# Performance work log

Measured on AMD Instinct MI355X. Metric: run time of the kernel, lower is better.

## Reference

```python
import jax, jax.numpy as jnp
import numpy as np

# Dimensions (source globals scaled to production: r=256 residues, s=128 sequences)
S, R, CM, CZ, C, H = 128, 256, 256, 128, 32, 8
EPS = 1e-5  # torch LayerNorm default


def setup_inputs() -> dict:
    key = jax.random.key(0)
    ks = jax.random.split(key, 14)
    msa = jax.random.normal(ks[0], (S, R, CM), dtype=jnp.float32)
    pair = jax.random.normal(ks[1], (R, R, CZ), dtype=jnp.float32)
    u = lambda k, shape, fan: jax.random.uniform(k, shape, jnp.float32, -1.0 / np.sqrt(fan), 1.0 / np.sqrt(fan))
    return {
        "msa": msa,
        "pair": pair,
        # per-head LayerNorm affine params (stacked over head axis)
        "ln_msa_g": 1.0 + 0.1 * jax.random.normal(ks[2], (H, CM), dtype=jnp.float32),
        "ln_msa_b": 0.1 * jax.random.normal(ks[3], (H, CM), dtype=jnp.float32),
        "ln_pair_g": 1.0 + 0.1 * jax.random.normal(ks[4], (H, CZ), dtype=jnp.float32),
        "ln_pair_b": 0.1 * jax.random.normal(ks[5], (H, CZ), dtype=jnp.float32),
        # per-head projections (torch Linear without bias; stored as (in, out))
        "Wq": u(ks[6], (H, CM, C), CM),
        "Wk": u(ks[7], (H, CM, C), CM),
        "Wv": u(ks[8], (H, CM, C), CM),
        "Wg": u(ks[9], (H, CM, C), CM),
        "Wb": u(ks[10], (H, CZ, S), CZ),  # linear_b: c_z -> s
        # output projection c*H -> c_m (with bias)
        "Wo": u(ks[11], (H * C, CM), H * C),
        "bo": u(ks[12], (CM,), H * C),
    }


def _forward(msa, pair, ln_msa_g, ln_msa_b, ln_pair_g, ln_pair_b, Wq, Wk, Wv, Wg, Wb, Wo, bo):
    # LayerNorm normalization is head-independent; only affine differs per head.
    mu = msa.mean(-1, keepdims=True)
    var = msa.var(-1, keepdims=True)
    nm = (msa - mu) * jax.lax.rsqrt(var + EPS)              # (S, R, CM)
    p = nm[None] * ln_msa_g[:, None, None, :] + ln_msa_b[:, None, None, :]  # (H, S, R, CM)

    q = jnp.einsum("hsrc,hcd->hsrd", p, Wq)                  # (H, S, R, C)
    k = jnp.einsum("hsrc,hcd->hsrd", p, Wk)
    v = jnp.einsum("hsrc,hcd->hsrd", p, Wv)
    g = jax.nn.sigmoid(jnp.einsum("hsrc,hcd->hsrd", p, Wg))

    pmu = pair.mean(-1, keepdims=True)
    pvar = pair.var(-1, keepdims=True)
    npair = (pair - pmu) * jax.lax.rsqrt(pvar + EPS)         # (R, R, CZ)
    pp = npair[None] * ln_pair_g[:, None, None, :] + ln_pair_b[:, None, None, :]  # (H, R, R, CZ)
    bflat = jnp.einsum("hijc,hcs->hijs", pp, Wb)             # (H, R, R, S)
    # Faithful to torch: b = linear_b(flat_pair).view(s, r, r) -- a raw
    # row-major reinterpretation (NOT a transpose).
    b = bflat.reshape(H, S, R, R)

    inv_sqrt_c = np.float32(1.0 / np.sqrt(C))
    scores = (jnp.einsum("hsid,hsjd->hsij", q, k) + b) * inv_sqrt_c  # (H, S, R, R)
    # Source softmax is over dim=-2 (the query/row axis), faithful here.
    a = jax.nn.softmax(scores, axis=-2)
    o = g * jnp.einsum("hsij,hsjd->hsid", a, v)              # (H, S, R, C)

    # concat heads on last dim: (S, R, H*C)
    cat = jnp.transpose(o, (1, 2, 0, 3)).reshape(S, R, H * C)
    return cat @ Wo + bo                                      # (S, R, CM)


def reference(msa, pair, ln_msa_g, ln_msa_b, ln_pair_g, ln_pair_b, Wq, Wk, Wv, Wg, Wb, Wo, bo):
    return _forward(msa, pair, ln_msa_g, ln_msa_b, ln_pair_g, ln_pair_b, Wq, Wk, Wv, Wg, Wb, Wo, bo)
```

## Files before the change

### kernel.cpp

```cpp
#include <hip/hip_runtime.h>
#include <hip/hip_bf16.h>


namespace {
constexpr int S_ = 128, R_ = 256, CM_ = 256, CZ_ = 128, C_ = 32, H_ = 8;
constexpr int SR_ = S_ * R_;
constexpr int RR_ = R_ * R_;
constexpr float EPS_ = 1e-5f;
constexpr float ISC_ = 0.17677669529663687f;

constexpr size_t OFF_WC  = 0;
constexpr size_t OFF_BC  = 131072;
constexpr size_t OFF_BBP = 132096;
constexpr size_t F32_END = 133120;
constexpr size_t BF_BASE = F32_END * 4;
constexpr size_t QKVG_ELEMS  = (size_t)H_ * SR_ * C_;
constexpr size_t CAT_ELEMS   = (size_t)SR_ * CM_;
constexpr size_t WBT_ELEMS   = (size_t)H_ * 128 * 128;
constexpr size_t WOT_ELEMS   = (size_t)256 * 256;
constexpr size_t PAIRN_ELEMS = (size_t)RR_ * 128;
constexpr size_t MSAN_ELEMS  = (size_t)SR_ * 256;
constexpr size_t NEED_BYTES =
    BF_BASE +
    (4 * QKVG_ELEMS + CAT_ELEMS + WBT_ELEMS + WOT_ELEMS + PAIRN_ELEMS + MSAN_ELEMS) * 2;
}

typedef unsigned short bf_t;
typedef short s8v __attribute__((ext_vector_type(8)));
typedef float f4v __attribute__((ext_vector_type(4)));

__device__ __forceinline__ unsigned pk2(float lo, float hi) {
  __hip_bfloat162 t = __float22bfloat162_rn(float2{lo, hi});
  return *reinterpret_cast<unsigned*>(&t);
}
__device__ __forceinline__ bf_t pk1(float v) {
  __hip_bfloat16 t = __float2bfloat16(v);
  return *reinterpret_cast<bf_t*>(&t);
}
__device__ __forceinline__ float uplo(unsigned u) { return __uint_as_float(u << 16); }
__device__ __forceinline__ f4v mfma16(s8v a, s8v b, f4v c) {
  return __builtin_amdgcn_mfma_f32_16x16x32_bf16(a, b, c, 0, 0, 0);
}
__device__ __forceinline__ s8v ld8(const bf_t* p) { return *reinterpret_cast<const s8v*>(p); }

__global__ __launch_bounds__(512) void prep_all_k(
    const float* __restrict__ pair, const float* __restrict__ msa,
    const float* __restrict__ lng_m, const float* __restrict__ lnb_m,
    const float* __restrict__ lng_p, const float* __restrict__ lnb_p,
    const float* __restrict__ Wq, const float* __restrict__ Wk, const float* __restrict__ Wv,
    const float* __restrict__ Wg, const float* __restrict__ Wb, const float* __restrict__ Wo,
    bf_t* __restrict__ pairN, bf_t* __restrict__ msaN, bf_t* __restrict__ wct,
    bf_t* __restrict__ wbt, bf_t* __restrict__ wot, float* __restrict__ bc,
    float* __restrict__ bbp) {
  int b = blockIdx.x;
  int tid = threadIdx.x;
  int lane = tid & 63;
  if (b < 8192) {
    int row = b * 8 + (tid >> 6);
    float2 v = reinterpret_cast<const float2*>(pair + (size_t)row * CZ_)[lane];
    float s = v.x + v.y;
    float s2 = v.x * v.x + v.y * v.y;
    for (int off = 32; off; off >>= 1) {
      s += __shfl_xor(s, off);
      s2 += __shfl_xor(s2, off);
    }
    float m = s / CZ_;
    float rs = rsqrtf(s2 / CZ_ - m * m + EPS_);
    reinterpret_cast<unsigned*>(pairN)[(size_t)row * 64 + lane] =
        pk2((v.x - m) * rs, (v.y - m) * rs);
  } else if (b < 12288) {
    int row = (b - 8192) * 8 + (tid >> 6);
    float4 v = reinterpret_cast<const float4*>(msa + (size_t)row * CM_)[lane];
    float s = v.x + v.y + v.z + v.w;
    float s2 = v.x * v.x + v.y * v.y + v.z * v.z + v.w * v.w;
    for (int off = 32; off; off >>= 1) {
      s += __shfl_xor(s, off);
      s2 += __shfl_xor(s2, off);
    }
    float m = s / CM_;
    float rs = rsqrtf(s2 / CM_ - m * m + EPS_);
    uint2 wv;
    wv.x = pk2((v.x - m) * rs, (v.y - m) * rs);
    wv.y = pk2((v.z - m) * rs, (v.w - m) * rs);
    reinterpret_cast<uint2*>(msaN)[(size_t)row * 64 + lane] = wv;
  } else if (b < 13184) {
    int idx = (b - 12288) * 512 + tid;
    if (idx < 262144) {
      int h = idx >> 15, rem = idx & 32767;
      int j = rem >> 8, c = rem & 255;
      int m = j >> 5, d = j & 31;
      const float* Wsrc = (m == 0) ? Wq : (m == 1) ? Wk : (m == 2) ? Wv : Wg;
      float scale = (m == 0) ? ISC_ : 1.0f;
      wct[idx] = pk1(lng_m[h * CM_ + c] * Wsrc[((size_t)h * CM_ + c) * C_ + d] * scale);
    } else if (idx < 262144 + 131072) {
      int i2 = idx - 262144;
      int h = i2 >> 14, rem = i2 & 16383;
      int t = rem >> 7, c = rem & 127;
      wbt[i2] = pk1(lng_p[h * CZ_ + c] * Wb[((size_t)h * CZ_ + c) * S_ + t] * ISC_);
    } else {
      int i3 = idx - 262144 - 131072;
      int n = i3 >> 8, k = i3 & 255;
      wot[i3] = pk1(Wo[(size_t)k * 256 + n]);
    }
  } else {
    int ob = (b - 13184) * 4 + (tid >> 7);
    int t = tid & 127;
    if (ob < H_) {
      int h = ob;
      int m = t >> 5, d = t & 31;
      const float* Wsrc = (m == 0) ? Wq : (m == 1) ? Wk : (m == 2) ? Wv : Wg;
      float scale = (m == 0) ? ISC_ : 1.0f;
      float bias = 0.f;
      for (int c = 0; c < CM_; c++)
        bias += lnb_m[h * CM_ + c] * Wsrc[((size_t)h * CM_ + c) * C_ + d];
      bc[h * 128 + t] = bias * scale;
    } else {
      int h = ob - H_;
      float bias = 0.f;
      for (int c = 0; c < CZ_; c++)
        bias += lnb_p[h * CZ_ + c] * Wb[((size_t)h * CZ_ + c) * S_ + t];
      bbp[h * 128 + t] = bias * ISC_;
    }
  }
}

__global__ __launch_bounds__(512, 1) void qkvg_mfma_k(
    const bf_t* __restrict__ msaN, const bf_t* __restrict__ wct, const float* __restrict__ bc,
    bf_t* __restrict__ q, bf_t* __restrict__ k, bf_t* __restrict__ v, bf_t* __restrict__ g) {
  __shared__ bf_t sm_a[128 * 256];
  __shared__ bf_t sm_w[128 * 256];
  int ib = blockIdx.x;
  int tid = threadIdx.x;
  int w = tid >> 6, l = tid & 63;
  int l15 = l & 15, l4 = l >> 4;
  int iw = w >> 2, jw = w & 3;
  int sr0 = ib * 128;
  int sx7 = l15 & 7;
#pragma unroll
  for (int rep = 0; rep < 8; rep++) {
    int flat = rep * 512 + tid;
    int row = flat >> 5, c = flat & 31;
    *reinterpret_cast<uint4*>(&sm_a[row * 256 + ((c ^ (row & 7)) << 3)]) =
        *reinterpret_cast<const uint4*>(msaN + (size_t)(sr0 + row) * 256 + c * 8);
  }
  for (int h = 0; h < H_; h++) {
    __syncthreads();
#pragma unroll
    for (int rep = 0; rep < 8; rep++) {
      int flat = rep * 512 + tid;
      int row = flat >> 5, c = flat & 31;
      *reinterpret_cast<uint4*>(&sm_w[row * 256 + ((c ^ (row & 7)) << 3)]) =
          *reinterpret_cast<const uint4*>(wct + ((size_t)h * 128 + row) * 256 + c * 8);
    }
    f4v acc[4][2];
#pragma unroll
    for (int jt = 0; jt < 2; jt++) {
      float bb = bc[h * 128 + jw * 32 + jt * 16 + l15];
#pragma unroll
      for (int it = 0; it < 4; it++) acc[it][jt] = f4v{bb, bb, bb, bb};
    }
    __syncthreads();
#pragma unroll
    for (int ks = 0; ks < 8; ks++) {
      int ch = ks * 4 + l4;
      s8v a[4], b[2];
#pragma unroll
      for (int it = 0; it < 4; it++)
        a[it] = ld8(&sm_a[(iw * 64 + it * 16 + l15) * 256 + ((ch ^ sx7) << 3)]);
#pragma unroll
      for (int jt = 0; jt < 2; jt++)
        b[jt] = ld8(&sm_w[(jw * 32 + jt * 16 + l15) * 256 + ((ch ^ sx7) << 3)]);
#pragma unroll
      for (int it = 0; it < 4; it++)
#pragma unroll
        for (int jt = 0; jt < 2; jt++) acc[it][jt] = mfma16(a[it], b[jt], acc[it][jt]);
    }
#pragma unroll
    for (int it = 0; it < 4; it++) {
#pragma unroll
      for (int jt = 0; jt < 2; jt++) {
        int j = jw * 32 + jt * 16 + l15;
        int m_ = j >> 5, d = j & 31;
        bf_t* dst = (m_ == 0) ? q : (m_ == 1) ? k : (m_ == 2) ? v : g;
#pragma unroll
        for (int r = 0; r < 4; r++) {
          int i = iw * 64 + it * 16 + l4 * 4 + r;
          float val = acc[it][jt][r];
          if (m_ == 3) val = 1.f / (1.f + __expf(-val));
          dst[((size_t)h * SR_ + sr0 + i) * C_ + d] = pk1(val);
        }
      }
    }
  }
}

__global__ __launch_bounds__(512, 1) void attn_mfma_k(
    const bf_t* __restrict__ pairN, const bf_t* __restrict__ wbt,
    const float* __restrict__ bbp, const bf_t* __restrict__ qg, const bf_t* __restrict__ kg,
    const bf_t* __restrict__ vg, const bf_t* __restrict__ gg, bf_t* __restrict__ cat) {
  __shared__ bf_t sm_pN[256 * 128];
  __shared__ bf_t sm_wt[64 * 128];
  __shared__ bf_t sm_p[256 * 64];
  __shared__ bf_t sm_vt[32 * 64];
  __shared__ float sm_redm[4 * 64];
  __shared__ float sm_reds[4 * 64];

  int b = blockIdx.x;
  int x = b & 7, t = b >> 3;
  int round = t >> 5, inner = t & 31;
  int sl = inner >> 3, h = inner & 7;
  int s = (round * 8 + x) * 4 + sl;

  int tid = threadIdx.x;
  int w = tid >> 6, l = tid & 63;
  int l15 = l & 15, l4 = l >> 4;
  int iw = w >> 1, jw = w & 1;
  int iw2 = w >> 1, dw = w & 1;
  int sx7 = l15 & 7;
  size_t base = ((size_t)h * SR_ + (size_t)s * R_) * C_;

  s8v qa[4];
#pragma unroll
  for (int it = 0; it < 4; it++)
    qa[it] = ld8(&qg[base + (size_t)(iw * 64 + it * 16 + l15) * C_ + l4 * 8]);

  f4v accO[4];
#pragma unroll
  for (int it = 0; it < 4; it++) accO[it] = f4v{0.f, 0.f, 0.f, 0.f};

  for (int p = 0; p < 2; p++) {
    __syncthreads();
#pragma unroll
    for (int rep = 0; rep < 8; rep++) {
      int flat = rep * 512 + tid;
      int row = flat >> 4, c = flat & 15;
      int gr = (2 * s + (row >> 7)) * 256 + 2 * (row & 127) + p;
      *reinterpret_cast<uint4*>(&sm_pN[row * 128 + ((c ^ (row & 7)) << 3)]) =
          *reinterpret_cast<const uint4*>(pairN + (size_t)gr * 128 + c * 8);
    }
    for (int jh = 0; jh < 2; jh++) {
      int j0 = p * 128 + jh * 64;
      s8v kb0 = ld8(&kg[base + (size_t)(j0 + jw * 32 + l15) * C_ + l4 * 8]);
      s8v kb1 = ld8(&kg[base + (size_t)(j0 + jw * 32 + 16 + l15) * C_ + l4 * 8]);
      __syncthreads();
      if (tid < 256) {
#pragma unroll
        for (int rep = 0; rep < 4; rep++) {
          int flat = rep * 256 + tid;
          int row = flat >> 4, c = flat & 15;
          *reinterpret_cast<uint4*>(&sm_wt[row * 128 + ((c ^ (row & 7)) << 3)]) =
              *reinterpret_cast<const uint4*>(wbt + ((size_t)h * 128 + jh * 64 + row) * 128 +
                                              c * 8);
        }
      } else {
        int t2 = tid - 256;
        int j = t2 >> 2, dc = t2 & 3;
        uint4 u = *reinterpret_cast<const uint4*>(vg + base + (size_t)(j0 + j) * C_ + dc * 8);
        unsigned uu[4] = {u.x, u.y, u.z, u.w};
#pragma unroll
        for (int e = 0; e < 8; e++) {
          int d = dc * 8 + e;
          bf_t val = (bf_t)((uu[e >> 1] >> ((e & 1) * 16)) & 0xffff);
          sm_vt[d * 64 + ((((j >> 3) ^ (d & 7)) << 3) + (j & 7))] = val;
        }
      }
      f4v acc[4][2];
      {
        float bb0 = bbp[h * 128 + jh * 64 + jw * 32 + l15];
        float bb1 = bbp[h * 128 + jh * 64 + jw * 32 + 16 + l15];
#pragma unroll
        for (int it = 0; it < 4; it++) {
          acc[it][0] = f4v{bb0, bb0, bb0, bb0};
          acc[it][1] = f4v{bb1, bb1, bb1, bb1};
        }
      }
      __syncthreads();
#pragma unroll
      for (int ks = 0; ks < 4; ks++) {
        int ch = (ks * 4 + l4);
        s8v a[4], b2[2];
#pragma unroll
        for (int it = 0; it < 4; it++)
          a[it] = ld8(&sm_pN[(iw * 64 + it * 16 + l15) * 128 + ((ch ^ sx7) << 3)]);
#pragma unroll
        for (int u = 0; u < 2; u++)
          b2[u] = ld8(&sm_wt[(jw * 32 + u * 16 + l15) * 128 + ((ch ^ sx7) << 3)]);
#pragma unroll
        for (int it = 0; it < 4; it++) {
          acc[it][0] = mfma16(a[it], b2[0], acc[it][0]);
          acc[it][1] = mfma16(a[it], b2[1], acc[it][1]);
        }
      }
#pragma unroll
      for (int it = 0; it < 4; it++) {
        acc[it][0] = mfma16(qa[it], kb0, acc[it][0]);
        acc[it][1] = mfma16(qa[it], kb1, acc[it][1]);
      }
      float fac[2], mloc[2];
#pragma unroll
      for (int u = 0; u < 2; u++) {
        float m0 = -1e30f;
#pragma unroll
        for (int it = 0; it < 4; it++)
#pragma unroll
          for (int r = 0; r < 4; r++) m0 = fmaxf(m0, acc[it][u][r]);
        m0 = fmaxf(m0, __shfl_xor(m0, 16));
        m0 = fmaxf(m0, __shfl_xor(m0, 32));
        float s0 = 0.f;
#pragma unroll
        for (int it = 0; it < 4; it++)
#pragma unroll
          for (int r = 0; r < 4; r++) {
            float e = __expf(acc[it][u][r] - m0);
            acc[it][u][r] = e;
            s0 += e;
          }
        s0 += __shfl_xor(s0, 16);
        s0 += __shfl_xor(s0, 32);
        mloc[u] = m0;
        if (l < 16) {
          sm_redm[iw * 64 + jw * 32 + u * 16 + l] = m0;
          sm_reds[iw * 64 + jw * 32 + u * 16 + l] = s0;
        }
      }
      __syncthreads();
#pragma unroll
      for (int u = 0; u < 2; u++) {
        int jc = jw * 32 + u * 16 + l15;
        float M = fmaxf(fmaxf(sm_redm[jc], sm_redm[64 + jc]),
                        fmaxf(sm_redm[128 + jc], sm_redm[192 + jc]));
        float tot = 0.f;
#pragma unroll
        for (int gx = 0; gx < 4; gx++)
          tot += sm_reds[gx * 64 + jc] * __expf(sm_redm[gx * 64 + jc] - M);
        fac[u] = __expf(mloc[u] - M) / tot;
#pragma unroll
        for (int it = 0; it < 4; it++)
#pragma unroll
          for (int r = 0; r < 4; r++) {
            int i = iw * 64 + it * 16 + l4 * 4 + r;
            sm_p[i * 64 + ((((jc >> 3) ^ (i & 7)) << 3) + (jc & 7))] =
                pk1(acc[it][u][r] * fac[u]);
          }
      }
      __syncthreads();
#pragma unroll
      for (int ks = 0; ks < 2; ks++) {
        int ch = ks * 4 + l4;
        s8v vb = ld8(&sm_vt[(dw * 16 + l15) * 64 + ((ch ^ sx7) << 3)]);
#pragma unroll
        for (int it = 0; it < 4; it++) {
          s8v pa = ld8(&sm_p[(iw2 * 64 + it * 16 + l15) * 64 + ((ch ^ sx7) << 3)]);
          accO[it] = mfma16(pa, vb, accO[it]);
        }
      }
    }
  }
#pragma unroll
  for (int it = 0; it < 4; it++) {
#pragma unroll
    for (int r = 0; r < 4; r++) {
      int i = iw2 * 64 + it * 16 + l4 * 4 + r;
      int d = dw * 16 + l15;
      float gf = uplo((unsigned)gg[base + (size_t)i * C_ + d]);
      cat[((size_t)s * R_ + i) * 256 + h * 32 + d] = pk1(accO[it][r] * gf);
    }
  }
}

__global__ __launch_bounds__(512, 1) void out_mfma_k(const bf_t* __restrict__ cat,
                                                     const bf_t* __restrict__ wot,
                                                     const float* __restrict__ bo,
                                                     float* __restrict__ out) {
  __shared__ bf_t sm_a[128 * 256];
  __shared__ bf_t sm_b[128 * 256];
  int ib = blockIdx.x;
  int tid = threadIdx.x;
  int w = tid >> 6, l = tid & 63;
  int l15 = l & 15, l4 = l >> 4, sx7 = l15 & 7;
  int iw = w >> 2, jw = w & 3;
  int sr0 = ib * 128;
#pragma unroll
  for (int rep = 0; rep < 8; rep++) {
    int flat = rep * 512 + tid;
    int row = flat >> 5, c = flat & 31;
    *reinterpret_cast<uint4*>(&sm_a[row * 256 + ((c ^ (row & 7)) << 3)]) =
        *reinterpret_cast<const uint4*>(cat + (size_t)(sr0 + row) * 256 + c * 8);
  }
  for (int nb = 0; nb < 2; nb++) {
    __syncthreads();
#pragma unroll
    for (int rep = 0; rep < 8; rep++) {
      int flat = rep * 512 + tid;
      int row = flat >> 5, c = flat & 31;
      *reinterpret_cast<uint4*>(&sm_b[row * 256 + ((c ^ (row & 7)) << 3)]) =
          *reinterpret_cast<const uint4*>(wot + (size_t)(nb * 128 + row) * 256 + c * 8);
    }
    f4v acc[4][2];
#pragma unroll
    for (int jt = 0; jt < 2; jt++) {
      float bb = bo[nb * 128 + jw * 32 + jt * 16 + l15];
#pragma unroll
      for (int it = 0; it < 4; it++) acc[it][jt] = f4v{bb, bb, bb, bb};
    }
    __syncthreads();
#pragma unroll
    for (int ks = 0; ks < 8; ks++) {
      int ch = ks * 4 + l4;
      s8v a[4], b[2];
#pragma unroll
      for (int it = 0; it < 4; it++)
        a[it] = ld8(&sm_a[(iw * 64 + it * 16 + l15) * 256 + ((ch ^ sx7) << 3)]);
#pragma unroll
      for (int jt = 0; jt < 2; jt++)
        b[jt] = ld8(&sm_b[(jw * 32 + jt * 16 + l15) * 256 + ((ch ^ sx7) << 3)]);
#pragma unroll
      for (int it = 0; it < 4; it++)
#pragma unroll
        for (int jt = 0; jt < 2; jt++) acc[it][jt] = mfma16(a[it], b[jt], acc[it][jt]);
    }
#pragma unroll
    for (int it = 0; it < 4; it++)
#pragma unroll
      for (int jt = 0; jt < 2; jt++) {
        int n = nb * 128 + jw * 32 + jt * 16 + l15;
#pragma unroll
        for (int r = 0; r < 4; r++) {
          int i = iw * 64 + it * 16 + l4 * 4 + r;
          out[(size_t)(sr0 + i) * 256 + n] = acc[it][jt][r];
        }
      }
  }
}

extern "C" void kernel_launch(void* const* d_in, const int* in_sizes, int n_in, void* d_out,
                              int out_size, void* d_ws, size_t ws_size, hipStream_t stream) {
  if (ws_size < NEED_BYTES) return;

  const float* msa = (const float*)d_in[0];
  const float* pair = (const float*)d_in[1];
  const float* lng_m = (const float*)d_in[2];
  const float* lnb_m = (const float*)d_in[3];
  const float* lng_p = (const float*)d_in[4];
  const float* lnb_p = (const float*)d_in[5];
  const float* Wq = (const float*)d_in[6];
  const float* Wk = (const float*)d_in[7];
  const float* Wv = (const float*)d_in[8];
  const float* Wg = (const float*)d_in[9];
  const float* Wb = (const float*)d_in[10];
  const float* Wo = (const float*)d_in[11];
  const float* bo = (const float*)d_in[12];
  float* out = (float*)d_out;
  float* ws = (float*)d_ws;

  bf_t* wct = (bf_t*)(ws + OFF_WC);
  float* bc = ws + OFF_BC;
  float* bbp = ws + OFF_BBP;
  bf_t* qb = (bf_t*)((char*)d_ws + BF_BASE);
  bf_t* kb = qb + QKVG_ELEMS;
  bf_t* vb = kb + QKVG_ELEMS;
  bf_t* gb = vb + QKVG_ELEMS;
  bf_t* cat = gb + QKVG_ELEMS;
  bf_t* wbt = cat + CAT_ELEMS;
  bf_t* wot = wbt + WBT_ELEMS;
  bf_t* pairN = wot + WOT_ELEMS;
  bf_t* msaN = pairN + PAIRN_ELEMS;

  prep_all_k<<<13188, 512, 0, stream>>>(pair, msa, lng_m, lnb_m, lng_p, lnb_p, Wq, Wk, Wv, Wg,
                                        Wb, Wo, pairN, msaN, wct, wbt, wot, bc, bbp);
  qkvg_mfma_k<<<SR_ / 128, 512, 0, stream>>>(msaN, wct, bc, qb, kb, vb, gb);
  attn_mfma_k<<<S_ * H_, 512, 0, stream>>>(pairN, wbt, bbp, qb, kb, vb, gb, cat);
  out_mfma_k<<<SR_ / 128, 512, 0, stream>>>(cat, wot, bo, out);
}
```

Measured before the change: 159.5 us.

## Shrink attention LDS footprint via K-chunked pair staging to raise occupancy

The attention kernel now stages the normalized pair tile and the Wb slice in two 64-channel K chunks instead of the full 128 channels. This cuts LDS use from about 96KB to about 48KB per block, and launch bounds are raised to allow more resident blocks per CU. The price is reloading the pair tile for every 64-column pass instead of once per 128-row parity, plus extra barriers. The prep kernel also moves the slow serial bias-reduction blocks to the front of the grid so they start early.

```diff
diff --git a/kernel.cpp b/kernel.cpp
--- a/kernel.cpp
+++ b/kernel.cpp
@@ -55,8 +55,27 @@
   int b = blockIdx.x;
   int tid = threadIdx.x;
   int lane = tid & 63;
-  if (b < 8192) {
-    int row = b * 8 + (tid >> 6);
+  if (b < 4) {
+    int ob = b * 4 + (tid >> 7);
+    int t = tid & 127;
+    if (ob < H_) {
+      int h = ob;
+      int m = t >> 5, d = t & 31;
+      const float* Wsrc = (m == 0) ? Wq : (m == 1) ? Wk : (m == 2) ? Wv : Wg;
+      float scale = (m == 0) ? ISC_ : 1.0f;
+      float bias = 0.f;
+      for (int c = 0; c < CM_; c++)
+        bias += lnb_m[h * CM_ + c] * Wsrc[((size_t)h * CM_ + c) * C_ + d];
+      bc[h * 128 + t] = bias * scale;
+    } else {
+      int h = ob - H_;
+      float bias = 0.f;
+      for (int c = 0; c < CZ_; c++)
+        bias += lnb_p[h * CZ_ + c] * Wb[((size_t)h * CZ_ + c) * S_ + t];
+      bbp[h * 128 + t] = bias * ISC_;
+    }
+  } else if (b < 8196) {
+    int row = (b - 4) * 8 + (tid >> 6);
     float2 v = reinterpret_cast<const float2*>(pair + (size_t)row * CZ_)[lane];
     float s = v.x + v.y;
     float s2 = v.x * v.x + v.y * v.y;
@@ -68,8 +87,8 @@
     float rs = rsqrtf(s2 / CZ_ - m * m + EPS_);
     reinterpret_cast<unsigned*>(pairN)[(size_t)row * 64 + lane] =
         pk2((v.x - m) * rs, (v.y - m) * rs);
-  } else if (b < 12288) {
-    int row = (b - 8192) * 8 + (tid >> 6);
+  } else if (b < 12292) {
+    int row = (b - 8196) * 8 + (tid >> 6);
     float4 v = reinterpret_cast<const float4*>(msa + (size_t)row * CM_)[lane];
     float s = v.x + v.y + v.z + v.w;
     float s2 = v.x * v.x + v.y * v.y + v.z * v.z + v.w * v.w;
@@ -83,8 +102,8 @@
     wv.x = pk2((v.x - m) * rs, (v.y - m) * rs);
     wv.y = pk2((v.z - m) * rs, (v.w - m) * rs);
     reinterpret_cast<uint2*>(msaN)[(size_t)row * 64 + lane] = wv;
-  } else if (b < 13184) {
-    int idx = (b - 12288) * 512 + tid;
+  } else {
+    int idx = (b - 12292) * 512 + tid;
     if (idx < 262144) {
       int h = idx >> 15, rem = idx & 32767;
       int j = rem >> 8, c = rem & 255;
@@ -102,25 +121,6 @@
       int n = i3 >> 8, k = i3 & 255;
       wot[i3] = pk1(Wo[(size_t)k * 256 + n]);
     }
-  } else {
-    int ob = (b - 13184) * 4 + (tid >> 7);
-    int t = tid & 127;
-    if (ob < H_) {
-      int h = ob;
-      int m = t >> 5, d = t & 31;
-      const float* Wsrc = (m == 0) ? Wq : (m == 1) ? Wk : (m == 2) ? Wv : Wg;
-      float scale = (m == 0) ? ISC_ : 1.0f;
-      float bias = 0.f;
-      for (int c = 0; c < CM_; c++)
-        bias += lnb_m[h * CM_ + c] * Wsrc[((size_t)h * CM_ + c) * C_ + d];
-      bc[h * 128 + t] = bias * scale;
-    } else {
-      int h = ob - H_;
-      float bias = 0.f;
-      for (int c = 0; c < CZ_; c++)
-        bias += lnb_p[h * CZ_ + c] * Wb[((size_t)h * CZ_ + c) * S_ + t];
-      bbp[h * 128 + t] = bias * ISC_;
-    }
   }
 }
 
@@ -194,30 +194,29 @@
   }
 }
 
-__global__ __launch_bounds__(512, 1) void attn_mfma_k(
+__global__ __launch_bounds__(512, 4) void attn_mfma_k(
     const bf_t* __restrict__ pairN, const bf_t* __restrict__ wbt,
     const float* __restrict__ bbp, const bf_t* __restrict__ qg, const bf_t* __restrict__ kg,
     const bf_t* __restrict__ vg, const bf_t* __restrict__ gg, bf_t* __restrict__ cat) {
-  __shared__ bf_t sm_pN[256 * 128];
-  __shared__ bf_t sm_wt[64 * 128];
+  __shared__ bf_t sm_pn[256 * 64];
+  __shared__ bf_t sm_wt[64 * 64];
   __shared__ bf_t sm_p[256 * 64];
   __shared__ bf_t sm_vt[32 * 64];
   __shared__ float sm_redm[4 * 64];
   __shared__ float sm_reds[4 * 64];
 
   int b = blockIdx.x;
-  int x = b & 7, t = b >> 3;
-  int round = t >> 5, inner = t & 31;
+  int x = b & 7, tq = b >> 3;
+  int round = tq >> 5, inner = tq & 31;
   int sl = inner >> 3, h = inner & 7;
   int s = (round * 8 + x) * 4 + sl;
 
   int tid = threadIdx.x;
   int w = tid >> 6, l = tid & 63;
-  int l15 = l & 15, l4 = l >> 4;
-  int iw = w >> 1, jw = w & 1;
-  int iw2 = w >> 1, dw = w & 1;
-  int sx7 = l15 & 7;
+  int l15 = l & 15, l4 = l >> 4, sx7 = l15 & 7;
+  int iw = w >> 1, jw = w & 1, dw = w & 1;
   size_t base = ((size_t)h * SR_ + (size_t)s * R_) * C_;
+  const bf_t* wbh = wbt + (size_t)h * 128 * 128;
 
   s8v qa[4];
 #pragma unroll
@@ -228,131 +227,130 @@
 #pragma unroll
   for (int it = 0; it < 4; it++) accO[it] = f4v{0.f, 0.f, 0.f, 0.f};
 
-  for (int p = 0; p < 2; p++) {
-    __syncthreads();
-#pragma unroll
-    for (int rep = 0; rep < 8; rep++) {
-      int flat = rep * 512 + tid;
-      int row = flat >> 4, c = flat & 15;
-      int gr = (2 * s + (row >> 7)) * 256 + 2 * (row & 127) + p;
-      *reinterpret_cast<uint4*>(&sm_pN[row * 128 + ((c ^ (row & 7)) << 3)]) =
-          *reinterpret_cast<const uint4*>(pairN + (size_t)gr * 128 + c * 8);
-    }
-    for (int jh = 0; jh < 2; jh++) {
-      int j0 = p * 128 + jh * 64;
-      s8v kb0 = ld8(&kg[base + (size_t)(j0 + jw * 32 + l15) * C_ + l4 * 8]);
-      s8v kb1 = ld8(&kg[base + (size_t)(j0 + jw * 32 + 16 + l15) * C_ + l4 * 8]);
+  for (int pass = 0; pass < 4; pass++) {
+    int p = pass >> 1, jh = pass & 1;
+    int j0 = p * 128 + jh * 64;
+    s8v kb0 = ld8(&kg[base + (size_t)(j0 + jw * 32 + l15) * C_ + l4 * 8]);
+    s8v kb1 = ld8(&kg[base + (size_t)(j0 + jw * 32 + 16 + l15) * C_ + l4 * 8]);
+    __syncthreads();
+    if (tid >= 256) {
+      int t2 = tid - 256;
+      int j = t2 >> 2, dc = t2 & 3;
+      uint4 u = *reinterpret_cast<const uint4*>(vg + base + (size_t)(j0 + j) * C_ + dc * 8);
+      unsigned uu[4] = {u.x, u.y, u.z, u.w};
+#pragma unroll
+      for (int e = 0; e < 8; e++) {
+        int d = dc * 8 + e;
+        bf_t val = (bf_t)((uu[e >> 1] >> ((e & 1) * 16)) & 0xffff);
+        sm_vt[d * 64 + ((((j >> 3) ^ (d & 7)) << 3) + (j & 7))] = val;
+      }
+    }
+    f4v acc[4][2];
+    {
+      float bb0 = bbp[h * 128 + jh * 64 + jw * 32 + l15];
+      float bb1 = bbp[h * 128 + jh * 64 + jw * 32 + 16 + l15];
+#pragma unroll
+      for (int it = 0; it < 4; it++) {
+        acc[it][0] = f4v{bb0, bb0, bb0, bb0};
+        acc[it][1] = f4v{bb1, bb1, bb1, bb1};
+      }
+    }
+#pragma unroll
+    for (int kc = 0; kc < 2; kc++) {
+#pragma unroll
+      for (int rep = 0; rep < 4; rep++) {
+        int idx = rep * 512 + tid;
+        int row = idx >> 3, c8 = idx & 7;
+        int gr = (2 * s + (row >> 7)) * 256 + 2 * (row & 127) + p;
+        *reinterpret_cast<uint4*>(&sm_pn[row * 64 + ((c8 ^ (row & 7)) << 3)]) =
+            *reinterpret_cast<const uint4*>(pairN + (size_t)gr * 128 + kc * 64 + c8 * 8);
+      }
+      {
+        int row = tid >> 3, c8 = tid & 7;
+        *reinterpret_cast<uint4*>(&sm_wt[row * 64 + ((c8 ^ (row & 7)) << 3)]) =
+            *reinterpret_cast<const uint4*>(wbh + (size_t)(jh * 64 + row) * 128 + kc * 64 +
+                                            c8 * 8);
+      }
       __syncthreads();
-      if (tid < 256) {
-#pragma unroll
-        for (int rep = 0; rep < 4; rep++) {
-          int flat = rep * 256 + tid;
-          int row = flat >> 4, c = flat & 15;
-          *reinterpret_cast<uint4*>(&sm_wt[row * 128 + ((c ^ (row & 7)) << 3)]) =
-              *reinterpret_cast<const uint4*>(wbt + ((size_t)h * 128 + jh * 64 + row) * 128 +
-                                              c * 8);
-        }
-      } else {
-        int t2 = tid - 256;
-        int j = t2 >> 2, dc = t2 & 3;
-        uint4 u = *reinterpret_cast<const uint4*>(vg + base + (size_t)(j0 + j) * C_ + dc * 8);
-        unsigned uu[4] = {u.x, u.y, u.z, u.w};
-#pragma unroll
-        for (int e = 0; e < 8; e++) {
-          int d = dc * 8 + e;
-          bf_t val = (bf_t)((uu[e >> 1] >> ((e & 1) * 16)) & 0xffff);
-          sm_vt[d * 64 + ((((j >> 3) ^ (d & 7)) << 3) + (j & 7))] = val;
-        }
-      }
-      f4v acc[4][2];
-      {
-        float bb0 = bbp[h * 128 + jh * 64 + jw * 32 + l15];
-        float bb1 = bbp[h * 128 + jh * 64 + jw * 32 + 16 + l15];
-#pragma unroll
-        for (int it = 0; it < 4; it++) {
-          acc[it][0] = f4v{bb0, bb0, bb0, bb0};
-          acc[it][1] = f4v{bb1, bb1, bb1, bb1};
-        }
-      }
-      __syncthreads();
-#pragma unroll
-      for (int ks = 0; ks < 4; ks++) {
-        int ch = (ks * 4 + l4);
+#pragma unroll
+      for (int ks = 0; ks < 2; ks++) {
+        int ch = ks * 4 + l4;
         s8v a[4], b2[2];
 #pragma unroll
         for (int it = 0; it < 4; it++)
-          a[it] = ld8(&sm_pN[(iw * 64 + it * 16 + l15) * 128 + ((ch ^ sx7) << 3)]);
+          a[it] = ld8(&sm_pn[(iw * 64 + it * 16 + l15) * 64 + ((ch ^ sx7) << 3)]);
 #pragma unroll
         for (int u = 0; u < 2; u++)
-          b2[u] = ld8(&sm_wt[(jw * 32 + u * 16 + l15) * 128 + ((ch ^ sx7) << 3)]);
+          b2[u] = ld8(&sm_wt[(jw * 32 + u * 16 + l15) * 64 + ((ch ^ sx7) << 3)]);
 #pragma unroll
         for (int it = 0; it < 4; it++) {
           acc[it][0] = mfma16(a[it], b2[0], acc[it][0]);
           acc[it][1] = mfma16(a[it], b2[1], acc[it][1]);
         }
       }
+      if (kc == 0) __syncthreads();
+    }
+#pragma unroll
+    for (int it = 0; it < 4; it++) {
+      acc[it][0] = mfma16(qa[it], kb0, acc[it][0]);
+      acc[it][1] = mfma16(qa[it], kb1, acc[it][1]);
+    }
+    float fac[2], mloc[2];
+#pragma unroll
+    for (int u = 0; u < 2; u++) {
+      float m0 = -1e30f;
+#pragma unroll
+      for (int it = 0; it < 4; it++)
+#pragma unroll
+        for (int r = 0; r < 4; r++) m0 = fmaxf(m0, acc[it][u][r]);
+      m0 = fmaxf(m0, __shfl_xor(m0, 16));
+      m0 = fmaxf(m0, __shfl_xor(m0, 32));
+      float s0 = 0.f;
+#pragma unroll
+      for (int it = 0; it < 4; it++)
+#pragma unroll
+        for (int r = 0; r < 4; r++) {
+          float e = __expf(acc[it][u][r] - m0);
+          acc[it][u][r] = e;
+          s0 += e;
+        }
+      s0 += __shfl_xor(s0, 16);
+      s0 += __shfl_xor(s0, 32);
+      mloc[u] = m0;
+      if (l < 16) {
+        sm_redm[iw * 64 + jw * 32 + u * 16 + l] = m0;
+        sm_reds[iw * 64 + jw * 32 + u * 16 + l] = s0;
+      }
+    }
+    __syncthreads();
+#pragma unroll
+    for (int u = 0; u < 2; u++) {
+      int jc = jw * 32 + u * 16 + l15;
+      float M = fmaxf(fmaxf(sm_redm[jc], sm_redm[64 + jc]),
+                      fmaxf(sm_redm[128 + jc], sm_redm[192 + jc]));
+      float tot = 0.f;
+#pragma unroll
+      for (int gx = 0; gx < 4; gx++)
+        tot += sm_reds[gx * 64 + jc] * __expf(sm_redm[gx * 64 + jc] - M);
+      fac[u] = __expf(mloc[u] - M) / tot;
+#pragma unroll
+      for (int it = 0; it < 4; it++)
+#pragma unroll
+        for (int r = 0; r < 4; r++) {
+          int i = iw * 64 + it * 16 + l4 * 4 + r;
+          sm_p[i * 64 + ((((jc >> 3) ^ (i & 7)) << 3) + (jc & 7))] =
+              pk1(acc[it][u][r] * fac[u]);
+        }
+    }
+    __syncthreads();
+#pragma unroll
+    for (int ks = 0; ks < 2; ks++) {
+      int ch = ks * 4 + l4;
+      s8v vb = ld8(&sm_vt[(dw * 16 + l15) * 64 + ((ch ^ sx7) << 3)]);
 #pragma unroll
       for (int it = 0; it < 4; it++) {
-        acc[it][0] = mfma16(qa[it], kb0, acc[it][0]);
-        acc[it][1] = mfma16(qa[it], kb1, acc[it][1]);
-      }
-      float fac[2], mloc[2];
-#pragma unroll
-      for (int u = 0; u < 2; u++) {
-        float m0 = -1e30f;
-#pragma unroll
-        for (int it = 0; it < 4; it++)
-#pragma unroll
-          for (int r = 0; r < 4; r++) m0 = fmaxf(m0, acc[it][u][r]);
-        m0 = fmaxf(m0, __shfl_xor(m0, 16));
-        m0 = fmaxf(m0, __shfl_xor(m0, 32));
-        float s0 = 0.f;
-#pragma unroll
-        for (int it = 0; it < 4; it++)
-#pragma unroll
-          for (int r = 0; r < 4; r++) {
-            float e = __expf(acc[it][u][r] - m0);
-            acc[it][u][r] = e;
-            s0 += e;
-          }
-        s0 += __shfl_xor(s0, 16);
-        s0 += __shfl_xor(s0, 32);
-        mloc[u] = m0;
-        if (l < 16) {
-          sm_redm[iw * 64 + jw * 32 + u * 16 + l] = m0;
-          sm_reds[iw * 64 + jw * 32 + u * 16 + l] = s0;
-        }
-      }
-      __syncthreads();
-#pragma unroll
-      for (int u = 0; u < 2; u++) {
-        int jc = jw * 32 + u * 16 + l15;
-        float M = fmaxf(fmaxf(sm_redm[jc], sm_redm[64 + jc]),
-                        fmaxf(sm_redm[128 + jc], sm_redm[192 + jc]));
-        float tot = 0.f;
-#pragma unroll
-        for (int gx = 0; gx < 4; gx++)
-          tot += sm_reds[gx * 64 + jc] * __expf(sm_redm[gx * 64 + jc] - M);
-        fac[u] = __expf(mloc[u] - M) / tot;
-#pragma unroll
-        for (int it = 0; it < 4; it++)
-#pragma unroll
-          for (int r = 0; r < 4; r++) {
-            int i = iw * 64 + it * 16 + l4 * 4 + r;
-            sm_p[i * 64 + ((((jc >> 3) ^ (i & 7)) << 3) + (jc & 7))] =
-                pk1(acc[it][u][r] * fac[u]);
-          }
-      }
-      __syncthreads();
-#pragma unroll
-      for (int ks = 0; ks < 2; ks++) {
-        int ch = ks * 4 + l4;
-        s8v vb = ld8(&sm_vt[(dw * 16 + l15) * 64 + ((ch ^ sx7) << 3)]);
-#pragma unroll
-        for (int it = 0; it < 4; it++) {
-          s8v pa = ld8(&sm_p[(iw2 * 64 + it * 16 + l15) * 64 + ((ch ^ sx7) << 3)]);
-          accO[it] = mfma16(pa, vb, accO[it]);
-        }
+        s8v pa = ld8(&sm_p[(iw * 64 + it * 16 + l15) * 64 + ((ch ^ sx7) << 3)]);
+        accO[it] = mfma16(pa, vb, accO[it]);
       }
     }
   }
@@ -360,7 +358,7 @@
   for (int it = 0; it < 4; it++) {
 #pragma unroll
     for (int r = 0; r < 4; r++) {
-      int i = iw2 * 64 + it * 16 + l4 * 4 + r;
+      int i = iw * 64 + it * 16 + l4 * 4 + r;
       int d = dw * 16 + l15;
       float gf = uplo((unsigned)gg[base + (size_t)i * C_ + d]);
       cat[((size_t)s * R_ + i) * 256 + h * 32 + d] = pk1(accO[it][r] * gf);
```

New measurement: 272.5 us. +70.8%, slower.

## Double attention block to 1024 threads and move bias blocks first in prep

Applied to the files above, without the earlier changes.

The attention kernel now runs 1024 threads (16 waves) per block. Each wave handles 32 query rows instead of 64, and the cross-wave softmax reduction spans 8 row groups. Loading of the Wb tile and the V transpose is redistributed across the larger thread count. Separately, the slow serial bias-dot-product blocks in the prep kernel are moved to the lowest block indices so they start first instead of trailing the launch. This is meant to add latency hiding and cut tail time, at the cost of more synchronisation participants and smaller MFMA tiles per wave.

```diff
diff --git a/kernel.cpp b/kernel.cpp
--- a/kernel.cpp
+++ b/kernel.cpp
@@ -55,8 +55,27 @@
   int b = blockIdx.x;
   int tid = threadIdx.x;
   int lane = tid & 63;
-  if (b < 8192) {
-    int row = b * 8 + (tid >> 6);
+  if (b < 4) {
+    int ob = b * 4 + (tid >> 7);
+    int t = tid & 127;
+    if (ob < H_) {
+      int h = ob;
+      int m = t >> 5, d = t & 31;
+      const float* Wsrc = (m == 0) ? Wq : (m == 1) ? Wk : (m == 2) ? Wv : Wg;
+      float scale = (m == 0) ? ISC_ : 1.0f;
+      float bias = 0.f;
+      for (int c = 0; c < CM_; c++)
+        bias += lnb_m[h * CM_ + c] * Wsrc[((size_t)h * CM_ + c) * C_ + d];
+      bc[h * 128 + t] = bias * scale;
+    } else {
+      int h = ob - H_;
+      float bias = 0.f;
+      for (int c = 0; c < CZ_; c++)
+        bias += lnb_p[h * CZ_ + c] * Wb[((size_t)h * CZ_ + c) * S_ + t];
+      bbp[h * 128 + t] = bias * ISC_;
+    }
+  } else if (b < 8196) {
+    int row = (b - 4) * 8 + (tid >> 6);
     float2 v = reinterpret_cast<const float2*>(pair + (size_t)row * CZ_)[lane];
     float s = v.x + v.y;
     float s2 = v.x * v.x + v.y * v.y;
@@ -68,8 +87,8 @@
     float rs = rsqrtf(s2 / CZ_ - m * m + EPS_);
     reinterpret_cast<unsigned*>(pairN)[(size_t)row * 64 + lane] =
         pk2((v.x - m) * rs, (v.y - m) * rs);
-  } else if (b < 12288) {
-    int row = (b - 8192) * 8 + (tid >> 6);
+  } else if (b < 12292) {
+    int row = (b - 8196) * 8 + (tid >> 6);
     float4 v = reinterpret_cast<const float4*>(msa + (size_t)row * CM_)[lane];
     float s = v.x + v.y + v.z + v.w;
     float s2 = v.x * v.x + v.y * v.y + v.z * v.z + v.w * v.w;
@@ -83,8 +102,8 @@
     wv.x = pk2((v.x - m) * rs, (v.y - m) * rs);
     wv.y = pk2((v.z - m) * rs, (v.w - m) * rs);
     reinterpret_cast<uint2*>(msaN)[(size_t)row * 64 + lane] = wv;
-  } else if (b < 13184) {
-    int idx = (b - 12288) * 512 + tid;
+  } else {
+    int idx = (b - 12292) * 512 + tid;
     if (idx < 262144) {
       int h = idx >> 15, rem = idx & 32767;
       int j = rem >> 8, c = rem & 255;
@@ -102,25 +121,6 @@
       int n = i3 >> 8, k = i3 & 255;
       wot[i3] = pk1(Wo[(size_t)k * 256 + n]);
     }
-  } else {
-    int ob = (b - 13184) * 4 + (tid >> 7);
-    int t = tid & 127;
-    if (ob < H_) {
-      int h = ob;
-      int m = t >> 5, d = t & 31;
-      const float* Wsrc = (m == 0) ? Wq : (m == 1) ? Wk : (m == 2) ? Wv : Wg;
-      float scale = (m == 0) ? ISC_ : 1.0f;
-      float bias = 0.f;
-      for (int c = 0; c < CM_; c++)
-        bias += lnb_m[h * CM_ + c] * Wsrc[((size_t)h * CM_ + c) * C_ + d];
-      bc[h * 128 + t] = bias * scale;
-    } else {
-      int h = ob - H_;
-      float bias = 0.f;
-      for (int c = 0; c < CZ_; c++)
-        bias += lnb_p[h * CZ_ + c] * Wb[((size_t)h * CZ_ + c) * S_ + t];
-      bbp[h * 128 + t] = bias * ISC_;
-    }
   }
 }
 
@@ -194,7 +194,7 @@
   }
 }
 
-__global__ __launch_bounds__(512, 1) void attn_mfma_k(
+__global__ __launch_bounds__(1024, 4) void attn_mfma_k(
     const bf_t* __restrict__ pairN, const bf_t* __restrict__ wbt,
     const float* __restrict__ bbp, const bf_t* __restrict__ qg, const bf_t* __restrict__ kg,
     const bf_t* __restrict__ vg, const bf_t* __restrict__ gg, bf_t* __restrict__ cat) {
@@ -202,37 +202,35 @@
   __shared__ bf_t sm_wt[64 * 128];
   __shared__ bf_t sm_p[256 * 64];
   __shared__ bf_t sm_vt[32 * 64];
-  __shared__ float sm_redm[4 * 64];
-  __shared__ float sm_reds[4 * 64];
+  __shared__ float sm_redm[8 * 64];
+  __shared__ float sm_reds[8 * 64];
 
   int b = blockIdx.x;
-  int x = b & 7, t = b >> 3;
-  int round = t >> 5, inner = t & 31;
+  int x = b & 7, tq = b >> 3;
+  int round = tq >> 5, inner = tq & 31;
   int sl = inner >> 3, h = inner & 7;
   int s = (round * 8 + x) * 4 + sl;
 
   int tid = threadIdx.x;
   int w = tid >> 6, l = tid & 63;
-  int l15 = l & 15, l4 = l >> 4;
-  int iw = w >> 1, jw = w & 1;
-  int iw2 = w >> 1, dw = w & 1;
-  int sx7 = l15 & 7;
+  int l15 = l & 15, l4 = l >> 4, sx7 = l15 & 7;
+  int iw = w >> 1, jw = w & 1, dw = w & 1;
   size_t base = ((size_t)h * SR_ + (size_t)s * R_) * C_;
 
-  s8v qa[4];
-#pragma unroll
-  for (int it = 0; it < 4; it++)
-    qa[it] = ld8(&qg[base + (size_t)(iw * 64 + it * 16 + l15) * C_ + l4 * 8]);
-
-  f4v accO[4];
-#pragma unroll
-  for (int it = 0; it < 4; it++) accO[it] = f4v{0.f, 0.f, 0.f, 0.f};
+  s8v qa[2];
+#pragma unroll
+  for (int it = 0; it < 2; it++)
+    qa[it] = ld8(&qg[base + (size_t)(iw * 32 + it * 16 + l15) * C_ + l4 * 8]);
+
+  f4v accO[2];
+#pragma unroll
+  for (int it = 0; it < 2; it++) accO[it] = f4v{0.f, 0.f, 0.f, 0.f};
 
   for (int p = 0; p < 2; p++) {
     __syncthreads();
 #pragma unroll
-    for (int rep = 0; rep < 8; rep++) {
-      int flat = rep * 512 + tid;
+    for (int rep = 0; rep < 4; rep++) {
+      int flat = rep * 1024 + tid;
       int row = flat >> 4, c = flat & 15;
       int gr = (2 * s + (row >> 7)) * 256 + 2 * (row & 127) + p;
       *reinterpret_cast<uint4*>(&sm_pN[row * 128 + ((c ^ (row & 7)) << 3)]) =
@@ -243,18 +241,14 @@
       s8v kb0 = ld8(&kg[base + (size_t)(j0 + jw * 32 + l15) * C_ + l4 * 8]);
       s8v kb1 = ld8(&kg[base + (size_t)(j0 + jw * 32 + 16 + l15) * C_ + l4 * 8]);
       __syncthreads();
+      {
+        int row = tid >> 4, c = tid & 15;
+        *reinterpret_cast<uint4*>(&sm_wt[row * 128 + ((c ^ (row & 7)) << 3)]) =
+            *reinterpret_cast<const uint4*>(wbt + ((size_t)h * 128 + jh * 64 + row) * 128 +
+                                            c * 8);
+      }
       if (tid < 256) {
-#pragma unroll
-        for (int rep = 0; rep < 4; rep++) {
-          int flat = rep * 256 + tid;
-          int row = flat >> 4, c = flat & 15;
-          *reinterpret_cast<uint4*>(&sm_wt[row * 128 + ((c ^ (row & 7)) << 3)]) =
-              *reinterpret_cast<const uint4*>(wbt + ((size_t)h * 128 + jh * 64 + row) * 128 +
-                                              c * 8);
-        }
-      } else {
-        int t2 = tid - 256;
-        int j = t2 >> 2, dc = t2 & 3;
+        int j = tid >> 2, dc = tid & 3;
         uint4 u = *reinterpret_cast<const uint4*>(vg + base + (size_t)(j0 + j) * C_ + dc * 8);
         unsigned uu[4] = {u.x, u.y, u.z, u.w};
 #pragma unroll
@@ -264,12 +258,12 @@
           sm_vt[d * 64 + ((((j >> 3) ^ (d & 7)) << 3) + (j & 7))] = val;
         }
       }
-      f4v acc[4][2];
+      f4v acc[2][2];
       {
         float bb0 = bbp[h * 128 + jh * 64 + jw * 32 + l15];
         float bb1 = bbp[h * 128 + jh * 64 + jw * 32 + 16 + l15];
 #pragma unroll
-        for (int it = 0; it < 4; it++) {
+        for (int it = 0; it < 2; it++) {
           acc[it][0] = f4v{bb0, bb0, bb0, bb0};
           acc[it][1] = f4v{bb1, bb1, bb1, bb1};
         }
@@ -278,21 +272,21 @@
 #pragma unroll
       for (int ks = 0; ks < 4; ks++) {
         int ch = (ks * 4 + l4);
-        s8v a[4], b2[2];
-#pragma unroll
-        for (int it = 0; it < 4; it++)
-          a[it] = ld8(&sm_pN[(iw * 64 + it * 16 + l15) * 128 + ((ch ^ sx7) << 3)]);
+        s8v a[2], b2[2];
+#pragma unroll
+        for (int it = 0; it < 2; it++)
+          a[it] = ld8(&sm_pN[(iw * 32 + it * 16 + l15) * 128 + ((ch ^ sx7) << 3)]);
 #pragma unroll
         for (int u = 0; u < 2; u++)
           b2[u] = ld8(&sm_wt[(jw * 32 + u * 16 + l15) * 128 + ((ch ^ sx7) << 3)]);
 #pragma unroll
-        for (int it = 0; it < 4; it++) {
+        for (int it = 0; it < 2; it++) {
           acc[it][0] = mfma16(a[it], b2[0], acc[it][0]);
           acc[it][1] = mfma16(a[it], b2[1], acc[it][1]);
         }
       }
 #pragma unroll
-      for (int it = 0; it < 4; it++) {
+      for (int it = 0; it < 2; it++) {
         acc[it][0] = mfma16(qa[it], kb0, acc[it][0]);
         acc[it][1] = mfma16(qa[it], kb1, acc[it][1]);
       }
@@ -301,14 +295,14 @@
       for (int u = 0; u < 2; u++) {
         float m0 = -1e30f;
 #pragma unroll
-        for (int it = 0; it < 4; it++)
+        for (int it = 0; it < 2; it++)
 #pragma unroll
           for (int r = 0; r < 4; r++) m0 = fmaxf(m0, acc[it][u][r]);
         m0 = fmaxf(m0, __shfl_xor(m0, 16));
         m0 = fmaxf(m0, __shfl_xor(m0, 32));
         float s0 = 0.f;
 #pragma unroll
-        for (int it = 0; it < 4; it++)
+        for (int it = 0; it < 2; it++)
 #pragma unroll
           for (int r = 0; r < 4; r++) {
             float e = __expf(acc[it][u][r] - m0);
@@ -327,18 +321,19 @@
 #pragma unroll
       for (int u = 0; u < 2; u++) {
         int jc = jw * 32 + u * 16 + l15;
-        float M = fmaxf(fmaxf(sm_redm[jc], sm_redm[64 + jc]),
-                        fmaxf(sm_redm[128 + jc], sm_redm[192 + jc]));
+        float M = -1e30f;
+#pragma unroll
+        for (int gx = 0; gx < 8; gx++) M = fmaxf(M, sm_redm[gx * 64 + jc]);
         float tot = 0.f;
 #pragma unroll
-        for (int gx = 0; gx < 4; gx++)
+        for (int gx = 0; gx < 8; gx++)
           tot += sm_reds[gx * 64 + jc] * __expf(sm_redm[gx * 64 + jc] - M);
         fac[u] = __expf(mloc[u] - M) / tot;
 #pragma unroll
-        for (int it = 0; it < 4; it++)
+        for (int it = 0; it < 2; it++)
 #pragma unroll
           for (int r = 0; r < 4; r++) {
-            int i = iw * 64 + it * 16 + l4 * 4 + r;
+            int i = iw * 32 + it * 16 + l4 * 4 + r;
             sm_p[i * 64 + ((((jc >> 3) ^ (i & 7)) << 3) + (jc & 7))] =
                 pk1(acc[it][u][r] * fac[u]);
           }
@@ -349,18 +344,18 @@
         int ch = ks * 4 + l4;
         s8v vb = ld8(&sm_vt[(dw * 16 + l15) * 64 + ((ch ^ sx7) << 3)]);
 #pragma unroll
-        for (int it = 0; it < 4; it++) {
-          s8v pa = ld8(&sm_p[(iw2 * 64 + it * 16 + l15) * 64 + ((ch ^ sx7) << 3)]);
+        for (int it = 0; it < 2; it++) {
+          s8v pa = ld8(&sm_p[(iw * 32 + it * 16 + l15) * 64 + ((ch ^ sx7) << 3)]);
           accO[it] = mfma16(pa, vb, accO[it]);
         }
       }
     }
   }
 #pragma unroll
-  for (int it = 0; it < 4; it++) {
+  for (int it = 0; it < 2; it++) {
 #pragma unroll
     for (int r = 0; r < 4; r++) {
-      int i = iw2 * 64 + it * 16 + l4 * 4 + r;
+      int i = iw * 32 + it * 16 + l4 * 4 + r;
       int d = dw * 16 + l15;
       float gf = uplo((unsigned)gg[base + (size_t)i * C_ + d]);
       cat[((size_t)s * R_ + i) * 256 + h * 32 + d] = pk1(accO[it][r] * gf);
@@ -469,6 +464,6 @@
   prep_all_k<<<13188, 512, 0, stream>>>(pair, msa, lng_m, lnb_m, lng_p, lnb_p, Wq, Wk, Wv, Wg,
                                         Wb, Wo, pairN, msaN, wct, wbt, wot, bc, bbp);
   qkvg_mfma_k<<<SR_ / 128, 512, 0, stream>>>(msaN, wct, bc, qb, kb, vb, gb);
-  attn_mfma_k<<<S_ * H_, 512, 0, stream>>>(pairN, wbt, bbp, qb, kb, vb, gb, cat);
+  attn_mfma_k<<<S_ * H_, 1024, 0, stream>>>(pairN, wbt, bbp, qb, kb, vb, gb, cat);
   out_mfma_k<<<SR_ / 128, 512, 0, stream>>>(cat, wot, bo, out);
 }
```

After: 212.6 us. +33.2%, slower.
